# Kernel optimization log

Hardware: AMD Instinct MI355X
Metric: run time of the kernel (lower is better)

The kernel has to match this reference:

```python
import jax, jax.numpy as jnp
import numpy as np

B, S, IN_D, OUT_D, QD = 4, 1024, 16, 16, 32
HID, HEADS, HD, L, TED = 256, 8, 32, 4, 256
DECAY = 0.1
SCALE = HD ** -0.5


def _ln(x):
    m = x.mean(-1, keepdims=True)
    v = ((x - m) ** 2).mean(-1, keepdims=True)
    return (x - m) * jax.lax.rsqrt(v + 1e-5)


def _lin(x, w, b):
    # torch nn.Linear: y = x @ W^T + b, W is [out, in]
    return jnp.einsum('...i,oi->...o', x, w) + b


def _sin_emb(t, dim):
    half = dim // 2
    freqs = jnp.exp(-np.log(10000.0) * jnp.arange(half, dtype=jnp.float32) / (half - 1))
    a = t[:, None] * freqs[None, :]
    return jnp.concatenate([jnp.sin(a), jnp.cos(a)], axis=-1)


def _mish(x):
    return x * jnp.tanh(jax.nn.softplus(x))


def _gelu(x):
    return jax.nn.gelu(x, approximate=False)


def setup_inputs() -> dict:
    key = jax.random.key(0)
    ks = iter(jax.random.split(key, 64))

    def w(shape):
        return jax.random.normal(next(ks), shape, dtype=jnp.float32) * 0.02

    d = {}
    d['x'] = jax.random.normal(next(ks), (B, S, IN_D), dtype=jnp.float32)
    d['query'] = jax.random.normal(next(ks), (B, QD), dtype=jnp.float32)
    d['time'] = jax.random.uniform(next(ks), (B,), dtype=jnp.float32) * 1000.0
    d['tm_w1'] = w((TED * 4, TED)); d['tm_b1'] = jnp.zeros((TED * 4,), jnp.float32)
    d['tm_w2'] = w((TED, TED * 4)); d['tm_b2'] = jnp.zeros((TED,), jnp.float32)
    d['in_w'] = w((HID, IN_D)); d['in_b'] = jnp.zeros((HID,), jnp.float32)
    d['q_w1'] = w((HID, QD)); d['q_b1'] = jnp.zeros((HID,), jnp.float32)
    d['q_w2'] = w((HID, HID)); d['q_b2'] = jnp.zeros((HID,), jnp.float32)
    d['n1_w'] = jnp.ones((L, HID), jnp.float32); d['n1_b'] = jnp.zeros((L, HID), jnp.float32)
    d['qkv_w'] = w((L, 3 * HID, HID)); d['qkv_b'] = jnp.zeros((L, 3 * HID), jnp.float32)
    d['ap_w'] = w((L, HID, HID)); d['ap_b'] = jnp.zeros((L, HID), jnp.float32)
    d['rel_bias'] = w((L, 2 * S - 1, HEADS))
    d['n2_w'] = jnp.ones((L, HID), jnp.float32); d['n2_b'] = jnp.zeros((L, HID), jnp.float32)
    d['f1_w'] = w((L, 4 * HID, HID)); d['f1_b'] = jnp.zeros((L, 4 * HID), jnp.float32)
    d['f2_w'] = w((L, HID, 4 * HID)); d['f2_b'] = jnp.zeros((L, HID), jnp.float32)
    d['t1_w'] = w((L, HID, TED)); d['t1_b'] = jnp.zeros((L, HID), jnp.float32)
    d['t2_w'] = w((L, HID, HID)); d['t2_b'] = jnp.zeros((L, HID), jnp.float32)
    d['out_w'] = w((OUT_D, HID)); d['out_b'] = jnp.zeros((OUT_D,), jnp.float32)
    return d


def reference(x, query, time, tm_w1, tm_b1, tm_w2, tm_b2, in_w, in_b,
              q_w1, q_b1, q_w2, q_b2, n1_w, n1_b, qkv_w, qkv_b, ap_w, ap_b,
              rel_bias, n2_w, n2_b, f1_w, f1_b, f2_w, f2_b, t1_w, t1_b,
              t2_w, t2_b, out_w, out_b):
    Bx, Sx, _ = x.shape
    # time MLP: SinusoidalPosEmb -> Linear -> Mish -> Linear
    te = _lin(_sin_emb(time, TED), tm_w1, tm_b1)
    te = _lin(_mish(te), tm_w2, tm_b2)            # [B, TED]
    # input projection + query conditioning (relative-pos path: no abs pos emb)
    h = _lin(x, in_w, in_b)                        # [B, S, HID]
    qe = _lin(_gelu(_lin(query, q_w1, q_b1)), q_w2, q_b2)
    h = h + qe[:, None, :]
    # shared relative-distance structures
    idx = jnp.arange(Sx)
    rel = idx[:, None] - idx[None, :]              # [S, S]
    dec = jnp.exp(-DECAY * jnp.abs(rel).astype(jnp.float32))
    rel_idx = rel + S - 1                          # index into 2*max_seq_len-1 table
    for l in range(L):
        # time conditioning per block
        tp = _lin(_gelu(_lin(te, t1_w[l], t1_b[l])), t2_w[l], t2_b[l])
        xn = _ln(h + tp[:, None, :]) * n1_w[l] + n1_b[l]
        qkv = _lin(xn, qkv_w[l], qkv_b[l]).reshape(Bx, Sx, 3, HEADS, HD)
        qkv = qkv.transpose(2, 0, 3, 1, 4)          # [3, B, H, S, hd]
        q_, k_, v_ = qkv[0], qkv[1], qkv[2]
        attn = jnp.einsum('bhqd,bhkd->bhqk', q_, k_) * SCALE
        bias = rel_bias[l][rel_idx]                 # [S, S, H]
        attn = attn + (dec[:, :, None] * bias).transpose(2, 0, 1)[None]
        a = jax.nn.softmax(attn, axis=-1)
        o = jnp.einsum('bhqk,bhkd->bhqd', a, v_)
        o = o.transpose(0, 2, 1, 3).reshape(Bx, Sx, HID)
        h = h + _lin(o, ap_w[l], ap_b[l])           # residual from pre-time x
        xn2 = _ln(h) * n2_w[l] + n2_b[l]
        h = h + _lin(_gelu(_lin(xn2, f1_w[l], f1_b[l])), f2_w[l], f2_b[l])
    return _lin(h, out_w, out_b)
```

## Files before the change

kernel.cpp:

```cpp
#include <hip/hip_runtime.h>
#include <hip/hip_bf16.h>
#include <math.h>

#define S_LEN 1024
#define HID 256
#define HEADS 8
#define HD 32
#define NLAYER 4
#define TED 256
#define BATCH 4
#define DECAY 0.1f
#define ATT_SCALE 0.17677669529663687f
#define LOG2E 1.4426950408889634f

typedef __bf16 bf8_t __attribute__((ext_vector_type(8)));
typedef float f4_t __attribute__((ext_vector_type(4)));

__device__ __forceinline__ float gelu_f(float x) {
  return 0.5f * x * (1.f + erff(x * 0.70710678118654752f));
}
__device__ __forceinline__ __bf16 f2bf(float f) { return (__bf16)f; }

__global__ __launch_bounds__(256) void k_boot(
    const float* __restrict__ s0, __bf16* __restrict__ d0,
    const float* __restrict__ s1, __bf16* __restrict__ d1,
    const float* __restrict__ s2, __bf16* __restrict__ d2,
    const float* __restrict__ s3, __bf16* __restrict__ d3,
    const float* __restrict__ relb, float* __restrict__ decb_t,
    const float* __restrict__ timev,
    const float* __restrict__ tm_w1, const float* __restrict__ tm_b1,
    const float* __restrict__ query,
    const float* __restrict__ q_w1, const float* __restrict__ q_b1,
    float* __restrict__ te1, float* __restrict__ q1) {
  int bid = blockIdx.x;
  int lane = threadIdx.x & 63;
  if (bid < 1536) {
    const float* s; __bf16* d; int base;
    if (bid < 384)       { s = s0; d = d0; base = bid; }
    else if (bid < 512)  { s = s1; d = d1; base = bid - 384; }
    else if (bid < 1024) { s = s2; d = d2; base = bid - 512; }
    else                 { s = s3; d = d3; base = bid - 1024; }
    int i = (base * 256 + threadIdx.x) * 8;
    float4 a = *(const float4*)(s + i);
    float4 b = *(const float4*)(s + i + 4);
    bf8_t o;
    o[0] = f2bf(a.x); o[1] = f2bf(a.y); o[2] = f2bf(a.z); o[3] = f2bf(a.w);
    o[4] = f2bf(b.x); o[5] = f2bf(b.y); o[6] = f2bf(b.z); o[7] = f2bf(b.w);
    *(bf8_t*)(d + i) = o;
  } else if (bid < 1792) {
    int lb = bid - 1536;
    int l = lb >> 6;
    int i = (lb & 63) * 256 + threadIdx.x;
    if (i < 2047 * 8) {
      int idx = i >> 3, hh = i & 7;
      float dec = __expf(-DECAY * fabsf((float)(idx - 1023)));
      decb_t[(l * 8 + hh) * 2048 + idx] = dec * relb[(size_t)l * 2047 * 8 + i] * LOG2E;
    }
  } else if (bid < 2816) {
    int r = (bid - 1792) * 4 + (threadIdx.x >> 6);
    int o = r & 1023, b = r >> 10;
    float t = timev[b];
    float ev[4];
#pragma unroll
    for (int e = 0; e < 4; e++) {
      int k = lane * 4 + e;
      int i = k & 127;
      float f = __expf(-logf(10000.f) * (float)i / 127.f);
      float a = t * f;
      ev[e] = (k < 128) ? sinf(a) : cosf(a);
    }
    float4 w4 = *(const float4*)(tm_w1 + (size_t)o * 256 + lane * 4);
    float s = ev[0] * w4.x + ev[1] * w4.y + ev[2] * w4.z + ev[3] * w4.w;
#pragma unroll
    for (int off = 32; off; off >>= 1) s += __shfl_xor(s, off);
    if (lane == 0) {
      s += tm_b1[o];
      float sp = (s > 20.f) ? s : log1pf(__expf(s));
      te1[r] = s * tanhf(sp);
    }
  } else {
    int r = (bid - 2816) * 4 + (threadIdx.x >> 6);
    int o = r & 255, b = r >> 8;
    float s = 0.f;
    if (lane < 8) {
      float4 a4 = *(const float4*)(query + b * 32 + lane * 4);
      float4 w4 = *(const float4*)(q_w1 + (size_t)o * 32 + lane * 4);
      s = a4.x * w4.x + a4.y * w4.y + a4.z * w4.z + a4.w * w4.w;
    }
#pragma unroll
    for (int off = 32; off; off >>= 1) s += __shfl_xor(s, off);
    if (lane == 0) q1[r] = gelu_f(s + q_b1[o]);
  }
}

__global__ __launch_bounds__(256) void k_prep_b(
    const float* __restrict__ te1, const float* __restrict__ tm_w2,
    const float* __restrict__ tm_b2,
    const float* __restrict__ q1, const float* __restrict__ q_w2,
    const float* __restrict__ q_b2,
    float* __restrict__ te, float* __restrict__ qe) {
  int bid = blockIdx.x;
  int lane = threadIdx.x & 63;
  bool iste = bid < 256;
  int r = (iste ? bid : bid - 256) * 4 + (threadIdx.x >> 6);
  int o = r & 255, b = r >> 8;
  int K = iste ? 1024 : 256;
  const float* a = (iste ? te1 : q1) + (size_t)b * K;
  const float* w = (iste ? tm_w2 : q_w2) + (size_t)o * K;
  float s = 0.f;
  for (int k = lane * 4; k < K; k += 256) {
    float4 a4 = *(const float4*)(a + k);
    float4 w4 = *(const float4*)(w + k);
    s += a4.x * w4.x + a4.y * w4.y + a4.z * w4.z + a4.w * w4.w;
  }
#pragma unroll
  for (int off = 32; off; off >>= 1) s += __shfl_xor(s, off);
  if (lane == 0) {
    s += (iste ? tm_b2 : q_b2)[o];
    (iste ? te : qe)[r] = s;
  }
}

__global__ __launch_bounds__(256) void k_mid(
    const float* __restrict__ te, const float* __restrict__ t1_w,
    const float* __restrict__ t1_b, float* __restrict__ tt,
    const float* __restrict__ x, const float* __restrict__ in_w,
    const float* __restrict__ in_b, const float* __restrict__ qe,
    float* __restrict__ h) {
  int bid = blockIdx.x;
  if (bid < 1024) {
    int r = bid * 4 + (threadIdx.x >> 6);
    int lane = threadIdx.x & 63;
    int o = r & 255;
    int b = (r >> 8) & 3;
    int g = r >> 10;
    float4 a4 = *(const float4*)(te + (size_t)b * 256 + lane * 4);
    float4 w4 = *(const float4*)(t1_w + ((size_t)(g * 256 + o)) * 256 + lane * 4);
    float s = a4.x * w4.x + a4.y * w4.y + a4.z * w4.z + a4.w * w4.w;
#pragma unroll
    for (int off = 32; off; off >>= 1) s += __shfl_xor(s, off);
    if (lane == 0) tt[r] = gelu_f(s + t1_b[g * 256 + o]);
  } else {
    int row = bid - 1024;
    int b = row >> 10;
    int j = threadIdx.x;
    __shared__ float xr[16];
    if (j < 16) xr[j] = x[row * 16 + j];
    __syncthreads();
    float s = in_b[j] + qe[b * 256 + j];
    const float* w = in_w + j * 16;
#pragma unroll
    for (int i = 0; i < 16; i++) s += xr[i] * w[i];
    h[(size_t)row * 256 + j] = s;
  }
}

__global__ __launch_bounds__(256) void k_t2(
    const float* __restrict__ tt, const float* __restrict__ t2_w,
    const float* __restrict__ t2_b, float* __restrict__ tp) {
  int r = blockIdx.x * 4 + (threadIdx.x >> 6);
  int lane = threadIdx.x & 63;
  int o = r & 255, b = (r >> 8) & 3, g = r >> 10;
  float4 a4 = *(const float4*)(tt + (size_t)(g * 4 + b) * 256 + lane * 4);
  float4 w4 = *(const float4*)(t2_w + (size_t)(g * 256 + o) * 256 + lane * 4);
  float s = a4.x * w4.x + a4.y * w4.y + a4.z * w4.z + a4.w * w4.w;
#pragma unroll
  for (int off = 32; off; off >>= 1) s += __shfl_xor(s, off);
  if (lane == 0) tp[r] = s + t2_b[g * 256 + o];
}

__global__ __launch_bounds__(256) void k_gemm_lnf(
    const float* __restrict__ h, const __bf16* __restrict__ W,
    const float* __restrict__ bias, __bf16* __restrict__ Cv,
    const float* __restrict__ tp, const float* __restrict__ lw,
    const float* __restrict__ lb) {
  constexpr int K = 256, BN = 128, NJ = 4, BQ = 2;
  const int N = 768;
  __shared__ __bf16 Al[64 * 264];
  __shared__ __bf16 Bl[2 * BN * 32];
  int tid = threadIdx.x;
  int w = tid >> 6, lane = tid & 63;
  int g = lane >> 4, c = lane & 15;
  int n0 = blockIdx.x * BN, m0 = blockIdx.y * 64;

  int srow = tid >> 2;
  int scol = (tid & 3) * 8;
  int sw = (((tid & 3) ^ ((tid >> 3) & 3))) * 8;
  const __bf16* Wb = W + (size_t)n0 * K + scol;
  bf8_t nB[2][BQ];
#pragma unroll
  for (int sub = 0; sub < 2; sub++)
#pragma unroll
    for (int q = 0; q < BQ; q++)
      nB[sub][q] = *(const bf8_t*)(Wb + (size_t)(q * 64 + srow) * K + sub * 32);

  int sub32 = tid & 31, lrow = tid >> 5;
  int colb = sub32 * 8;
  float4 lw0 = *(const float4*)(lw + colb), lw1 = *(const float4*)(lw + colb + 4);
  float4 lb0 = *(const float4*)(lb + colb), lb1 = *(const float4*)(lb + colb + 4);
  const float* tpr = tp + (m0 >> 10) * 256 + colb;
  float4 tp0 = *(const float4*)tpr, tp1 = *(const float4*)(tpr + 4);
#pragma unroll
  for (int p = 0; p < 8; p++) {
    int row = p * 8 + lrow;
    const float* hr = h + (size_t)(m0 + row) * 256 + colb;
    float4 a = *(const float4*)hr;
    float4 b2 = *(const float4*)(hr + 4);
    a.x += tp0.x; a.y += tp0.y; a.z += tp0.z; a.w += tp0.w;
    b2.x += tp1.x; b2.y += tp1.y; b2.z += tp1.z; b2.w += tp1.w;
    float sum = a.x + a.y + a.z + a.w + b2.x + b2.y + b2.z + b2.w;
    float ss = a.x * a.x + a.y * a.y + a.z * a.z + a.w * a.w +
               b2.x * b2.x + b2.y * b2.y + b2.z * b2.z + b2.w * b2.w;
#pragma unroll
    for (int m = 1; m < 32; m <<= 1) {
      sum += __shfl_xor(sum, m);
      ss += __shfl_xor(ss, m);
    }
    float mean = sum * (1.f / 256.f);
    float var = ss * (1.f / 256.f) - mean * mean;
    float rs = rsqrtf(var + 1e-5f);
    bf8_t o;
    o[0] = f2bf((a.x - mean) * rs * lw0.x + lb0.x);
    o[1] = f2bf((a.y - mean) * rs * lw0.y + lb0.y);
    o[2] = f2bf((a.z - mean) * rs * lw0.z + lb0.z);
    o[3] = f2bf((a.w - mean) * rs * lw0.w + lb0.w);
    o[4] = f2bf((b2.x - mean) * rs * lw1.x + lb1.x);
    o[5] = f2bf((b2.y - mean) * rs * lw1.y + lb1.y);
    o[6] = f2bf((b2.z - mean) * rs * lw1.z + lb1.z);
    o[7] = f2bf((b2.w - mean) * rs * lw1.w + lb1.w);
    *(bf8_t*)&Al[row * 264 + colb] = o;
  }

  int wr = (w >> 1) * 32, wc = (w & 1) * (BN / 2);
  int aseg = ((g ^ ((c >> 1) & 3))) * 8;
  f4_t acc[2][NJ];
#pragma unroll
  for (int i = 0; i < 2; i++)
#pragma unroll
    for (int j = 0; j < NJ; j++) acc[i][j] = (f4_t){0.f, 0.f, 0.f, 0.f};

#pragma unroll
  for (int ph = 0; ph < 4; ph++) {
    __syncthreads();
#pragma unroll
    for (int sub = 0; sub < 2; sub++)
#pragma unroll
      for (int q = 0; q < BQ; q++)
        *(bf8_t*)&Bl[sub * BN * 32 + (q * 64 + srow) * 32 + sw] = nB[sub][q];
    __syncthreads();
    if (ph < 3) {
#pragma unroll
      for (int sub = 0; sub < 2; sub++)
#pragma unroll
        for (int q = 0; q < BQ; q++)
          nB[sub][q] = *(const bf8_t*)(Wb + (size_t)(q * 64 + srow) * K +
                                       (ph + 1) * 64 + sub * 32);
    }
#pragma unroll
    for (int sub = 0; sub < 2; sub++) {
      bf8_t af[2], bfr[NJ];
#pragma unroll
      for (int i = 0; i < 2; i++)
        af[i] = *(const bf8_t*)&Al[(wr + i * 16 + c) * 264 + ph * 64 + sub * 32 + g * 8];
#pragma unroll
      for (int j = 0; j < NJ; j++)
        bfr[j] = *(const bf8_t*)&Bl[sub * BN * 32 + (wc + j * 16 + c) * 32 + aseg];
#pragma unroll
      for (int i = 0; i < 2; i++)
#pragma unroll
        for (int j = 0; j < NJ; j++)
          acc[i][j] = __builtin_amdgcn_mfma_f32_16x16x32_bf16(af[i], bfr[j], acc[i][j], 0, 0, 0);
    }
  }
#pragma unroll
  for (int j = 0; j < NJ; j++) {
    int col = n0 + wc + j * 16 + c;
    float bv = bias[col];
#pragma unroll
    for (int i = 0; i < 2; i++) {
#pragma unroll
      for (int rr = 0; rr < 4; rr++) {
        int row = m0 + wr + i * 16 + 4 * g + rr;
        Cv[(size_t)row * N + col] = f2bf(acc[i][j][rr] + bv);
      }
    }
  }
}

__global__ __launch_bounds__(256) void k_attn(
    const __bf16* __restrict__ qkv, const float* __restrict__ decb_t,
    __bf16* __restrict__ obuf) {
  __shared__ __bf16 Kl[128 * 40];
  __shared__ __bf16 Vt[32 * 136];
  __shared__ __bf16 Pl[4][16 * 136];
  __shared__ float db[1088];

  int tid = threadIdx.x;
  int w = tid >> 6, lane = tid & 63;
  int g = lane >> 4, c = lane & 15;
  int bh = blockIdx.y;
  int b = bh >> 3, hh = bh & 7;
  int q0 = blockIdx.x * 64;

  for (int i = tid; i < 1087; i += 256) db[i] = decb_t[hh * 2048 + q0 + i];

  bf8_t qraw = *(const bf8_t*)(qkv + ((size_t)(b * S_LEN + q0 + w * 16 + c)) * 768 + hh * 32 + 8 * g);
  bf8_t qfrag;
#pragma unroll
  for (int i = 0; i < 8; i++) qfrag[i] = f2bf((float)qraw[i] * (ATT_SCALE * LOG2E));

  float ps_acc[4] = {0.f, 0.f, 0.f, 0.f};
  f4_t o0 = {0.f, 0.f, 0.f, 0.f}, o1 = {0.f, 0.f, 0.f, 0.f};

  int rowb = w * 16 + 4 * g;
  __bf16* Plw = &Pl[w][0];

  int kvr = tid & 127;
  int part = tid >> 7;
  const __bf16* base0 = qkv + ((size_t)(b * S_LEN + kvr)) * 768 + hh * 32 + part * 16;
  bf8_t k8a = *(const bf8_t*)(base0 + 256);
  bf8_t k8b = *(const bf8_t*)(base0 + 264);
  bf8_t v8a = *(const bf8_t*)(base0 + 512);
  bf8_t v8b = *(const bf8_t*)(base0 + 520);

  for (int c0 = 0; c0 < S_LEN; c0 += 128) {
    __syncthreads();
    {
      *(bf8_t*)&Kl[kvr * 40 + part * 16] = k8a;
      *(bf8_t*)&Kl[kvr * 40 + part * 16 + 8] = k8b;
      int d0s = part * 16;
#pragma unroll
      for (int jj = 0; jj < 8; jj++) Vt[(d0s + jj) * 136 + kvr] = v8a[jj];
#pragma unroll
      for (int jj = 0; jj < 8; jj++) Vt[(d0s + 8 + jj) * 136 + kvr] = v8b[jj];
    }
    __syncthreads();
    if (c0 + 128 < S_LEN) {
      const __bf16* basen = base0 + (size_t)(c0 + 128) * 768;
      k8a = *(const bf8_t*)(basen + 256);
      k8b = *(const bf8_t*)(basen + 264);
      v8a = *(const bf8_t*)(basen + 512);
      v8b = *(const bf8_t*)(basen + 520);
    }

    f4_t sc[8];
    f4_t zero4 = {0.f, 0.f, 0.f, 0.f};
    __builtin_amdgcn_s_setprio(1);
#pragma unroll
    for (int j = 0; j < 8; j++) {
      bf8_t kfrag = *(const bf8_t*)&Kl[(j * 16 + c) * 40 + g * 8];
      sc[j] = __builtin_amdgcn_mfma_f32_16x16x32_bf16(qfrag, kfrag, zero4, 0, 0, 0);
    }
    __builtin_amdgcn_s_setprio(0);
#pragma unroll
    for (int j = 0; j < 8; j++) {
      int bidx = rowb + 1023 - (c0 + j * 16 + c);
#pragma unroll
      for (int r = 0; r < 4; r++) {
        float p = exp2f(sc[j][r] + db[bidx + r]);
        ps_acc[r] += p;
        Plw[(4 * g + r) * 136 + j * 16 + c] = f2bf(p);
      }
    }
    __builtin_amdgcn_s_setprio(1);
#pragma unroll
    for (int ss = 0; ss < 4; ss++) {
      bf8_t pa = *(const bf8_t*)&Plw[c * 136 + ss * 32 + g * 8];
      bf8_t v0 = *(const bf8_t*)&Vt[c * 136 + ss * 32 + g * 8];
      bf8_t v1 = *(const bf8_t*)&Vt[(c + 16) * 136 + ss * 32 + g * 8];
      o0 = __builtin_amdgcn_mfma_f32_16x16x32_bf16(pa, v0, o0, 0, 0, 0);
      o1 = __builtin_amdgcn_mfma_f32_16x16x32_bf16(pa, v1, o1, 0, 0, 0);
    }
    __builtin_amdgcn_s_setprio(0);
  }

#pragma unroll
  for (int r = 0; r < 4; r++) {
#pragma unroll
    for (int m = 1; m < 16; m <<= 1) ps_acc[r] += __shfl_xor(ps_acc[r], m);
    float inv = 1.f / ps_acc[r];
    size_t rowg = (size_t)(b * S_LEN + q0 + rowb + r);
    obuf[rowg * 256 + hh * 32 + c] = f2bf(o0[r] * inv);
    obuf[rowg * 256 + hh * 32 + 16 + c] = f2bf(o1[r] * inv);
  }
}

template <int NEXT>
__global__ __launch_bounds__(512) void k_back(
    const __bf16* __restrict__ obb, float* __restrict__ h,
    const __bf16* __restrict__ wap, const float* __restrict__ apb,
    const float* __restrict__ n2w, const float* __restrict__ n2b,
    const __bf16* __restrict__ wf1, const float* __restrict__ f1b,
    const __bf16* __restrict__ wf2, const float* __restrict__ f2b,
    const __bf16* __restrict__ wqkvn, const float* __restrict__ qkvbn,
    const float* __restrict__ tpn, const float* __restrict__ n1wn,
    const float* __restrict__ n1bn, __bf16* __restrict__ qkvb,
    const float* __restrict__ out_w, const float* __restrict__ out_b,
    float* __restrict__ out) {
  __shared__ __align__(16) char smem[108032];
  __bf16* Asm = (__bf16*)smem;
  __bf16* Bl  = (__bf16*)(smem + 8448);
  __bf16* y1l = (__bf16*)(smem + 73984);
  float (*red)[8][2] = (float(*)[8][2])(smem + 107008);

  int tid = threadIdx.x;
  int w = tid >> 6, lane = tid & 63;
  int g = lane >> 4, c = lane & 15;
  int m0 = blockIdx.x * 16;
  int srow = tid >> 2;
  int scol = (tid & 3) * 8;
  int sw = (((tid & 3) ^ ((srow >> 1) & 3))) * 8;
  int wc = w * 32;
  int axor = (c >> 1) & 3;
  int boff0 = (wc + c) * 32 + ((g ^ axor)) * 8;
  int boff1 = (wc + 16 + c) * 32 + ((g ^ axor)) * 8;
  int col0 = wc + c, col1 = wc + 16 + c;
  f4_t zero4 = {0.f, 0.f, 0.f, 0.f};

  bf8_t nB[4][2];
  auto prefetch = [&](const __bf16* base, int K, int ko) {
#pragma unroll
    for (int s = 0; s < 4; s++)
#pragma unroll
      for (int q = 0; q < 2; q++)
        nB[s][q] = *(const bf8_t*)(base + (size_t)(q * 128 + srow) * K + ko + s * 32 + scol);
  };
  auto stageB = [&]() {
    __syncthreads();
#pragma unroll
    for (int s = 0; s < 4; s++)
#pragma unroll
      for (int q = 0; q < 2; q++)
        *(bf8_t*)&Bl[s * 8192 + (q * 128 + srow) * 32 + sw] = nB[s][q];
    __syncthreads();
  };
  f4_t a0, a1;
  auto mstep = [&](const __bf16* Ab, int AS, int ko) {
#pragma unroll
    for (int s = 0; s < 4; s++) {
      bf8_t af = *(const bf8_t*)&Ab[c * AS + ko + s * 32 + g * 8];
      bf8_t b0 = *(const bf8_t*)&Bl[s * 8192 + boff0];
      bf8_t b1 = *(const bf8_t*)&Bl[s * 8192 + boff1];
      a0 = __builtin_amdgcn_mfma_f32_16x16x32_bf16(af, b0, a0, 0, 0, 0);
      a1 = __builtin_amdgcn_mfma_f32_16x16x32_bf16(af, b1, a1, 0, 0, 0);
    }
  };

  prefetch(wap, 256, 0);
  {
    int row = tid >> 5, gr = tid & 31;
    *(bf8_t*)&Asm[row * 264 + gr * 8] = *(const bf8_t*)(obb + (size_t)(m0 + row) * 256 + gr * 8);
  }
  a0 = zero4; a1 = zero4;
#pragma unroll
  for (int ph = 0; ph < 2; ph++) {
    stageB();
    if (ph == 0) prefetch(wap, 256, 128);
    else prefetch(wf1, 256, 0);
    mstep(Asm, 264, ph * 128);
  }

  float hn[2][4];
  {
    float b0v = apb[col0], b1v = apb[col1];
    float ps[4], pq[4];
#pragma unroll
    for (int r = 0; r < 4; r++) {
      size_t row = (size_t)(m0 + 4 * g + r);
      float v0 = a0[r] + b0v + h[row * 256 + col0];
      float v1 = a1[r] + b1v + h[row * 256 + col1];
      h[row * 256 + col0] = v0;
      h[row * 256 + col1] = v1;
      hn[0][r] = v0; hn[1][r] = v1;
      ps[r] = v0 + v1;
      pq[r] = v0 * v0 + v1 * v1;
    }
#pragma unroll
    for (int r = 0; r < 4; r++) {
#pragma unroll
      for (int m = 1; m < 16; m <<= 1) {
        ps[r] += __shfl_xor(ps[r], m);
        pq[r] += __shfl_xor(pq[r], m);
      }
    }
    if (c == 0) {
#pragma unroll
      for (int r = 0; r < 4; r++) {
        red[4 * g + r][w][0] = ps[r];
        red[4 * g + r][w][1] = pq[r];
      }
    }
  }
  __syncthreads();
  {
    float n2w0 = n2w[col0], n2b0 = n2b[col0];
    float n2w1 = n2w[col1], n2b1 = n2b[col1];
#pragma unroll
    for (int r = 0; r < 4; r++) {
      int row = 4 * g + r;
      float S = 0.f, Q = 0.f;
#pragma unroll
      for (int ww = 0; ww < 8; ww++) { S += red[row][ww][0]; Q += red[row][ww][1]; }
      float mean = S * (1.f / 256.f);
      float var = Q * (1.f / 256.f) - mean * mean;
      float rs = rsqrtf(var + 1e-5f);
      Asm[row * 264 + col0] = f2bf((hn[0][r] - mean) * rs * n2w0 + n2b0);
      Asm[row * 264 + col1] = f2bf((hn[1][r] - mean) * rs * n2w1 + n2b1);
    }
  }

#pragma unroll
  for (int nc = 0; nc < 4; nc++) {
    a0 = zero4; a1 = zero4;
#pragma unroll
    for (int ph = 0; ph < 2; ph++) {
      stageB();
      if (ph == 0) prefetch(wf1 + nc * 65536, 256, 128);
      else if (nc < 3) prefetch(wf1 + (nc + 1) * 65536, 256, 0);
      else prefetch(wf2, 1024, 0);
      mstep(Asm, 264, ph * 128);
    }
    float b0v = f1b[nc * 256 + col0], b1v = f1b[nc * 256 + col1];
#pragma unroll
    for (int r = 0; r < 4; r++) {
      y1l[(4 * g + r) * 1032 + nc * 256 + col0] = f2bf(gelu_f(a0[r] + b0v));
      y1l[(4 * g + r) * 1032 + nc * 256 + col1] = f2bf(gelu_f(a1[r] + b1v));
    }
  }

  a0 = zero4; a1 = zero4;
#pragma unroll
  for (int ph = 0; ph < 8; ph++) {
    stageB();
    if (ph < 7) prefetch(wf2, 1024, (ph + 1) * 128);
    else if (NEXT == 1) prefetch(wqkvn, 256, 0);
    mstep(y1l, 1032, ph * 128);
  }

  float hf[2][4];
  {
    float b0v = f2b[col0], b1v = f2b[col1];
#pragma unroll
    for (int r = 0; r < 4; r++) {
      size_t row = (size_t)(m0 + 4 * g + r);
      float v0 = h[row * 256 + col0] + a0[r] + b0v;
      float v1 = h[row * 256 + col1] + a1[r] + b1v;
      h[row * 256 + col0] = v0;
      h[row * 256 + col1] = v1;
      hf[0][r] = v0; hf[1][r] = v1;
    }
  }

  if (NEXT == 1) {
    int bb = m0 >> 10;
    float t0 = tpn[bb * 256 + col0], t1 = tpn[bb * 256 + col1];
    float v0r[4], v1r[4];
    {
      float ps[4], pq[4];
#pragma unroll
      for (int r = 0; r < 4; r++) {
        float v0 = hf[0][r] + t0, v1 = hf[1][r] + t1;
        v0r[r] = v0; v1r[r] = v1;
        ps[r] = v0 + v1;
        pq[r] = v0 * v0 + v1 * v1;
      }
#pragma unroll
      for (int r = 0; r < 4; r++) {
#pragma unroll
        for (int m = 1; m < 16; m <<= 1) {
          ps[r] += __shfl_xor(ps[r], m);
          pq[r] += __shfl_xor(pq[r], m);
        }
      }
      __syncthreads();
      if (c == 0) {
#pragma unroll
        for (int r = 0; r < 4; r++) {
          red[4 * g + r][w][0] = ps[r];
          red[4 * g + r][w][1] = pq[r];
        }
      }
    }
    __syncthreads();
    {
      float w0 = n1wn[col0], b0 = n1bn[col0];
      float w1 = n1wn[col1], b1 = n1bn[col1];
#pragma unroll
      for (int r = 0; r < 4; r++) {
        int row = 4 * g + r;
        float S = 0.f, Q = 0.f;
#pragma unroll
        for (int ww = 0; ww < 8; ww++) { S += red[row][ww][0]; Q += red[row][ww][1]; }
        float mean = S * (1.f / 256.f);
        float var = Q * (1.f / 256.f) - mean * mean;
        float rs = rsqrtf(var + 1e-5f);
        Asm[row * 264 + col0] = f2bf((v0r[r] - mean) * rs * w0 + b0);
        Asm[row * 264 + col1] = f2bf((v1r[r] - mean) * rs * w1 + b1);
      }
    }
#pragma unroll
    for (int nc = 0; nc < 3; nc++) {
      a0 = zero4; a1 = zero4;
#pragma unroll
      for (int ph = 0; ph < 2; ph++) {
        stageB();
        if (ph == 0) prefetch(wqkvn + nc * 65536, 256, 128);
        else if (nc < 2) prefetch(wqkvn + (nc + 1) * 65536, 256, 0);
        mstep(Asm, 264, ph * 128);
      }
      float b0v = qkvbn[nc * 256 + col0], b1v = qkvbn[nc * 256 + col1];
#pragma unroll
      for (int r = 0; r < 4; r++) {
        size_t row = (size_t)(m0 + 4 * g + r);
        qkvb[row * 768 + nc * 256 + col0] = f2bf(a0[r] + b0v);
        qkvb[row * 768 + nc * 256 + col1] = f2bf(a1[r] + b1v);
      }
    }
  } else if (NEXT == 2) {
    float* hl = (float*)(smem + 8448);
    __syncthreads();
#pragma unroll
    for (int r = 0; r < 4; r++) {
      int row = 4 * g + r;
      hl[row * 260 + col0] = hf[0][r];
      hl[row * 260 + col1] = hf[1][r];
    }
    __syncthreads();
    if (tid < 256) {
      int r = tid >> 4, cc = tid & 15;
      const float4* hr = (const float4*)&hl[r * 260];
      const float4* w4 = (const float4*)(out_w + cc * 256);
      float s = out_b[cc];
#pragma unroll 8
      for (int k = 0; k < 64; k++) {
        float4 a = hr[k], b = w4[k];
        s += a.x * b.x + a.y * b.y + a.z * b.z + a.w * b.w;
      }
      out[(m0 + r) * 16 + cc] = s;
    }
  }
}

extern "C" void kernel_launch(void* const* d_in, const int* in_sizes, int n_in,
                              void* d_out, int out_size, void* d_ws, size_t ws_size,
                              hipStream_t stream) {
  const float* x      = (const float*)d_in[0];
  const float* query  = (const float*)d_in[1];
  const float* timev  = (const float*)d_in[2];
  const float* tm_w1  = (const float*)d_in[3];
  const float* tm_b1  = (const float*)d_in[4];
  const float* tm_w2  = (const float*)d_in[5];
  const float* tm_b2  = (const float*)d_in[6];
  const float* in_w   = (const float*)d_in[7];
  const float* in_b   = (const float*)d_in[8];
  const float* q_w1   = (const float*)d_in[9];
  const float* q_b1   = (const float*)d_in[10];
  const float* q_w2   = (const float*)d_in[11];
  const float* q_b2   = (const float*)d_in[12];
  const float* n1_w   = (const float*)d_in[13];
  const float* n1_b   = (const float*)d_in[14];
  const float* qkv_w  = (const float*)d_in[15];
  const float* qkv_b  = (const float*)d_in[16];
  const float* ap_w   = (const float*)d_in[17];
  const float* ap_b   = (const float*)d_in[18];
  const float* relb   = (const float*)d_in[19];
  const float* n2_w   = (const float*)d_in[20];
  const float* n2_b   = (const float*)d_in[21];
  const float* f1_w   = (const float*)d_in[22];
  const float* f1_b   = (const float*)d_in[23];
  const float* f2_w   = (const float*)d_in[24];
  const float* f2_b   = (const float*)d_in[25];
  const float* t1_w   = (const float*)d_in[26];
  const float* t1_b   = (const float*)d_in[27];
  const float* t2_w   = (const float*)d_in[28];
  const float* t2_b   = (const float*)d_in[29];
  const float* out_w  = (const float*)d_in[30];
  const float* out_b  = (const float*)d_in[31];
  float* out = (float*)d_out;

  float* ws = (float*)d_ws;
  float*  h    = ws;
  __bf16* qkvb = (__bf16*)(ws + 1572864);
  __bf16* obb  = (__bf16*)(ws + 3145728);
  __bf16* wqkv = (__bf16*)(ws + 5767168);
  __bf16* wap  = (__bf16*)(ws + 6160384);
  __bf16* wf1  = (__bf16*)(ws + 6291456);
  __bf16* wf2  = (__bf16*)(ws + 6815744);
  float* decb  = ws + 7340032;
  float* qe    = decb + 65536;
  float* tp    = qe + 1024;
  float* te1   = tp + 4096;
  float* te    = te1 + 4096;
  float* q1    = te + 1024;
  float* tt    = q1 + 1024;

  k_boot<<<3072, 256, 0, stream>>>(qkv_w, wqkv, ap_w, wap, f1_w, wf1, f2_w, wf2,
                                   relb, decb, timev, tm_w1, tm_b1,
                                   query, q_w1, q_b1, te1, q1);
  k_prep_b<<<512, 256, 0, stream>>>(te1, tm_w2, tm_b2, q1, q_w2, q_b2, te, qe);
  k_mid<<<5120, 256, 0, stream>>>(te, t1_w, t1_b, tt, x, in_w, in_b, qe, h);
  k_t2<<<1024, 256, 0, stream>>>(tt, t2_w, t2_b, tp);

  k_gemm_lnf<<<dim3(6, 64), 256, 0, stream>>>(
      h, wqkv, qkv_b, qkvb, tp, n1_w, n1_b);

  for (int l = 0; l < NLAYER; l++) {
    k_attn<<<dim3(16, 32), 256, 0, stream>>>(qkvb, decb + l * 16384, obb);
    if (l < NLAYER - 1) {
      k_back<1><<<256, 512, 0, stream>>>(
          obb, h, wap + (size_t)l * 65536, ap_b + l * 256,
          n2_w + l * 256, n2_b + l * 256,
          wf1 + (size_t)l * 262144, f1_b + l * 1024,
          wf2 + (size_t)l * 262144, f2_b + l * 256,
          wqkv + (size_t)(l + 1) * 196608, qkv_b + (l + 1) * 768,
          tp + (l + 1) * 1024, n1_w + (l + 1) * 256, n1_b + (l + 1) * 256, qkvb,
          nullptr, nullptr, nullptr);
    } else {
      k_back<2><<<256, 512, 0, stream>>>(
          obb, h, wap + (size_t)l * 65536, ap_b + l * 256,
          n2_w + l * 256, n2_b + l * 256,
          wf1 + (size_t)l * 262144, f1_b + l * 1024,
          wf2 + (size_t)l * 262144, f2_b + l * 256,
          nullptr, nullptr, nullptr, nullptr, nullptr, nullptr,
          out_w, out_b, out);
    }
  }
}
```

Baseline: 267.6 us.

## Read weight fragments directly from global memory in k_back, drop LDS staging

Removes the register-prefetch and LDS staging of weight tiles in k_back. Each lane now loads its B fragments straight from global memory (relying on L2/L1 caching), and explicit barriers are added only between the phases that share LDS. This shrinks shared memory from about 108KB to about 42KB and sets launch bounds to 2 blocks, so more blocks can be resident per CU and many per-step barriers go away. The cost is that prefetch overlap is lost and global weight loads become strided per lane, which adds latency and cache pressure.

```diff
diff --git a/kernel.cpp b/kernel.cpp
--- a/kernel.cpp
+++ b/kernel.cpp
@@ -386,7 +386,7 @@
 }
 
 template <int NEXT>
-__global__ __launch_bounds__(512) void k_back(
+__global__ __launch_bounds__(512, 2) void k_back(
     const __bf16* __restrict__ obb, float* __restrict__ h,
     const __bf16* __restrict__ wap, const float* __restrict__ apb,
     const float* __restrict__ n2w, const float* __restrict__ n2b,
@@ -397,68 +397,39 @@
     const float* __restrict__ n1bn, __bf16* __restrict__ qkvb,
     const float* __restrict__ out_w, const float* __restrict__ out_b,
     float* __restrict__ out) {
-  __shared__ __align__(16) char smem[108032];
+  __shared__ __align__(16) char smem[42496];
   __bf16* Asm = (__bf16*)smem;
-  __bf16* Bl  = (__bf16*)(smem + 8448);
-  __bf16* y1l = (__bf16*)(smem + 73984);
-  float (*red)[8][2] = (float(*)[8][2])(smem + 107008);
+  __bf16* y1l = (__bf16*)(smem + 8448);
+  float (*red)[8][2] = (float(*)[8][2])(smem + 41472);
 
   int tid = threadIdx.x;
   int w = tid >> 6, lane = tid & 63;
   int g = lane >> 4, c = lane & 15;
   int m0 = blockIdx.x * 16;
-  int srow = tid >> 2;
-  int scol = (tid & 3) * 8;
-  int sw = (((tid & 3) ^ ((srow >> 1) & 3))) * 8;
   int wc = w * 32;
-  int axor = (c >> 1) & 3;
-  int boff0 = (wc + c) * 32 + ((g ^ axor)) * 8;
-  int boff1 = (wc + 16 + c) * 32 + ((g ^ axor)) * 8;
   int col0 = wc + c, col1 = wc + 16 + c;
   f4_t zero4 = {0.f, 0.f, 0.f, 0.f};
-
-  bf8_t nB[4][2];
-  auto prefetch = [&](const __bf16* base, int K, int ko) {
-#pragma unroll
-    for (int s = 0; s < 4; s++)
-#pragma unroll
-      for (int q = 0; q < 2; q++)
-        nB[s][q] = *(const bf8_t*)(base + (size_t)(q * 128 + srow) * K + ko + s * 32 + scol);
-  };
-  auto stageB = [&]() {
-    __syncthreads();
-#pragma unroll
-    for (int s = 0; s < 4; s++)
-#pragma unroll
-      for (int q = 0; q < 2; q++)
-        *(bf8_t*)&Bl[s * 8192 + (q * 128 + srow) * 32 + sw] = nB[s][q];
-    __syncthreads();
-  };
   f4_t a0, a1;
-  auto mstep = [&](const __bf16* Ab, int AS, int ko) {
-#pragma unroll
-    for (int s = 0; s < 4; s++) {
-      bf8_t af = *(const bf8_t*)&Ab[c * AS + ko + s * 32 + g * 8];
-      bf8_t b0 = *(const bf8_t*)&Bl[s * 8192 + boff0];
-      bf8_t b1 = *(const bf8_t*)&Bl[s * 8192 + boff1];
+
+  auto gloop = [&](const __bf16* Ab, int AS, int ko_a, const __bf16* W0,
+                   const __bf16* W1, int K) {
+    for (int ks = 0; ks < K; ks += 32) {
+      bf8_t af = *(const bf8_t*)&Ab[c * AS + ko_a + ks + g * 8];
+      bf8_t b0 = *(const bf8_t*)(W0 + ks + g * 8);
+      bf8_t b1 = *(const bf8_t*)(W1 + ks + g * 8);
       a0 = __builtin_amdgcn_mfma_f32_16x16x32_bf16(af, b0, a0, 0, 0, 0);
       a1 = __builtin_amdgcn_mfma_f32_16x16x32_bf16(af, b1, a1, 0, 0, 0);
     }
   };
 
-  prefetch(wap, 256, 0);
   {
     int row = tid >> 5, gr = tid & 31;
     *(bf8_t*)&Asm[row * 264 + gr * 8] = *(const bf8_t*)(obb + (size_t)(m0 + row) * 256 + gr * 8);
   }
+  __syncthreads();
+
   a0 = zero4; a1 = zero4;
-#pragma unroll
-  for (int ph = 0; ph < 2; ph++) {
-    stageB();
-    if (ph == 0) prefetch(wap, 256, 128);
-    else prefetch(wf1, 256, 0);
-    mstep(Asm, 264, ph * 128);
-  }
+  gloop(Asm, 264, 0, wap + (size_t)col0 * 256, wap + (size_t)col1 * 256, 256);
 
   float hn[2][4];
   {
@@ -508,18 +479,13 @@
       Asm[row * 264 + col1] = f2bf((hn[1][r] - mean) * rs * n2w1 + n2b1);
     }
   }
+  __syncthreads();
 
 #pragma unroll
   for (int nc = 0; nc < 4; nc++) {
     a0 = zero4; a1 = zero4;
-#pragma unroll
-    for (int ph = 0; ph < 2; ph++) {
-      stageB();
-      if (ph == 0) prefetch(wf1 + nc * 65536, 256, 128);
-      else if (nc < 3) prefetch(wf1 + (nc + 1) * 65536, 256, 0);
-      else prefetch(wf2, 1024, 0);
-      mstep(Asm, 264, ph * 128);
-    }
+    gloop(Asm, 264, 0, wf1 + (size_t)(nc * 256 + col0) * 256,
+          wf1 + (size_t)(nc * 256 + col1) * 256, 256);
     float b0v = f1b[nc * 256 + col0], b1v = f1b[nc * 256 + col1];
 #pragma unroll
     for (int r = 0; r < 4; r++) {
@@ -527,15 +493,10 @@
       y1l[(4 * g + r) * 1032 + nc * 256 + col1] = f2bf(gelu_f(a1[r] + b1v));
     }
   }
+  __syncthreads();
 
   a0 = zero4; a1 = zero4;
-#pragma unroll
-  for (int ph = 0; ph < 8; ph++) {
-    stageB();
-    if (ph < 7) prefetch(wf2, 1024, (ph + 1) * 128);
-    else if (NEXT == 1) prefetch(wqkvn, 256, 0);
-    mstep(y1l, 1032, ph * 128);
-  }
+  gloop(y1l, 1032, 0, wf2 + (size_t)col0 * 1024, wf2 + (size_t)col1 * 1024, 1024);
 
   float hf[2][4];
   {
@@ -598,16 +559,12 @@
         Asm[row * 264 + col1] = f2bf((v1r[r] - mean) * rs * w1 + b1);
       }
     }
+    __syncthreads();
 #pragma unroll
     for (int nc = 0; nc < 3; nc++) {
       a0 = zero4; a1 = zero4;
-#pragma unroll
-      for (int ph = 0; ph < 2; ph++) {
-        stageB();
-        if (ph == 0) prefetch(wqkvn + nc * 65536, 256, 128);
-        else if (nc < 2) prefetch(wqkvn + (nc + 1) * 65536, 256, 0);
-        mstep(Asm, 264, ph * 128);
-      }
+      gloop(Asm, 264, 0, wqkvn + (size_t)(nc * 256 + col0) * 256,
+            wqkvn + (size_t)(nc * 256 + col1) * 256, 256);
       float b0v = qkvbn[nc * 256 + col0], b1v = qkvbn[nc * 256 + col1];
 #pragma unroll
       for (int r = 0; r < 4; r++) {
```

Result: slower. 329.1 us (+23.0%).
